# Kernel tuning notes

Measured on AMD Instinct MI355X. Metric: run time of the kernel, lower is better.

## Reference

```python
import jax, jax.numpy as jnp
import numpy as np
import math

HEAD_DIM = 128
NUM_HEADS = 16
ROPE_BASE = 10000.0


def _rope(x, st_pos):
    # x: [B, S, H, hd], interleaved even/odd rotation as in the torch module
    S, hd = x.shape[1], x.shape[3]
    theta = 1.0 / (ROPE_BASE ** (jnp.arange(0, hd, 2, dtype=jnp.float32) / hd))  # [hd/2]
    pos = jnp.arange(st_pos, st_pos + S, dtype=jnp.float32)[:, None]             # [S,1]
    ang = pos * theta                                                            # [S, hd/2]
    sin = jnp.sin(ang)[None, :, None, :]
    cos = jnp.cos(ang)[None, :, None, :]
    xe, xo = x[..., 0::2], x[..., 1::2]
    re = xe * cos - xo * sin
    ro = xe * sin + xo * cos
    # re-interleave: stack pairs then flatten last two dims
    return jnp.stack([re, ro], axis=-1).reshape(x.shape)


def setup_inputs() -> dict:
    key = jax.random.key(0)
    ks = jax.random.split(key, 6)
    B, S, D = 4, 2048, 2048
    scale = 1.0 / math.sqrt(D)
    x = jax.random.normal(ks[0], (B, S, D), dtype=jnp.float32)
    # causal additive mask (prefill)
    mask = jnp.where(jnp.tril(jnp.ones((S, S), dtype=bool)), 0.0, -1e9).astype(jnp.float32)
    Wq = jax.random.normal(ks[1], (D, NUM_HEADS * HEAD_DIM), dtype=jnp.float32) * scale
    Wk = jax.random.normal(ks[2], (D, NUM_HEADS * HEAD_DIM), dtype=jnp.float32) * scale
    Wv = jax.random.normal(ks[3], (D, NUM_HEADS * HEAD_DIM), dtype=jnp.float32) * scale
    Wo = jax.random.normal(ks[4], (NUM_HEADS * HEAD_DIM, D), dtype=jnp.float32) * scale
    return {"x": x, "mask": mask, "Wq": Wq, "Wk": Wk, "Wv": Wv, "Wo": Wo, "st_pos": 0}


def reference(x, mask, Wq, Wk, Wv, Wo, st_pos):
    B, S, D = x.shape
    H, hd = NUM_HEADS, HEAD_DIM
    q = (x @ Wq).reshape(B, S, H, hd)
    k = (x @ Wk).reshape(B, S, H, hd)
    v = (x @ Wv).reshape(B, S, H, hd)
    q = _rope(q, st_pos)
    k = _rope(k, st_pos)
    # st_pos=0 prefill: cache slice == current k, v; n_rep == 1 (n_kv_heads=num_heads)
    scores = jnp.einsum('bqhd,bkhd->bhqk', q, k) / math.sqrt(hd)
    if mask is not None:
        scores = scores + mask
    attn = jax.nn.softmax(scores, axis=-1)
    a = jnp.einsum('bhqk,bkhd->bqhd', attn, v).reshape(B, S, H * hd)
    return a @ Wo
```

## Files before the change

kernel.cpp:

```cpp
#include <hip/hip_runtime.h>
#include <hip/hip_fp16.h>

typedef _Float16 f16;
typedef __attribute__((ext_vector_type(2))) _Float16 f16x2;
typedef __attribute__((ext_vector_type(4))) _Float16 f16x4v;
typedef __attribute__((ext_vector_type(8))) _Float16 f16x8;
typedef __attribute__((ext_vector_type(4))) float f32x4;
typedef __attribute__((ext_vector_type(4))) int i32x4;

#define DEV __device__ __forceinline__

static constexpr int S_ = 2048;
static constexpr int D_ = 2048;
static constexpr int H_ = 16;
static constexpr int HD_ = 128;
static constexpr int B_ = 4;
static constexpr int QKV_ST = 6144;

typedef const __attribute__((address_space(1))) void* gptr_t;
typedef __attribute__((address_space(3))) void* lptr_t;

DEV void gl_lds16(const void* gsrc, void* lds) {
  __builtin_amdgcn_global_load_lds((gptr_t)gsrc, (lptr_t)lds, 16, 0, 0);
}

DEV int cvt_pk_i32(float a, float b) {
  return __builtin_bit_cast(int, __builtin_amdgcn_cvt_pkrtz(a, b));
}

__global__ __launch_bounds__(256) void cvt_f32_to_f16(const float* __restrict__ in,
                                                      f16* __restrict__ out, long n) {
  long i0 = ((long)blockIdx.x * 256 + threadIdx.x) * 4;
  long stride = (long)gridDim.x * 256 * 4;
  for (long i = i0; i < n; i += stride) {
    float4 v = *(const float4*)(in + i);
    f16x4v o;
    o[0] = (f16)v.x; o[1] = (f16)v.y; o[2] = (f16)v.z; o[3] = (f16)v.w;
    *(f16x4v*)(out + i) = o;
  }
}

__global__ __launch_bounds__(256) void wtrans4(const float* __restrict__ W0, const float* __restrict__ W1,
                                               const float* __restrict__ W2, const float* __restrict__ W3,
                                               f16* __restrict__ Wt) {
  __shared__ float tile[32][33];
  int wi = blockIdx.y;
  const float* W = wi == 0 ? W0 : wi == 1 ? W1 : wi == 2 ? W2 : W3;
  f16* dst = Wt + (size_t)wi * D_ * D_;
  int bx = blockIdx.x & 63, by = blockIdx.x >> 6;
  int r0 = by << 5, c0 = bx << 5;
  int tx = threadIdx.x & 31, ty = threadIdx.x >> 5;
#pragma unroll
  for (int i = 0; i < 4; i++) {
    int r = ty + i * 8;
    tile[r][tx] = W[(size_t)(r0 + r) * D_ + c0 + tx];
  }
  __syncthreads();
#pragma unroll
  for (int i = 0; i < 4; i++) {
    int r = ty + i * 8;
    dst[(size_t)(c0 + r) * D_ + r0 + tx] = (f16)tile[tx][r];
  }
}

DEV f16x8 lds_frag(const f16* half, int row, int s, int lg) {
  int byte = row * 128 + s * 64 + lg * 16;
  byte ^= (row & 7) << 4;
  return *(const f16x8*)((const char*)half + byte);
}

template <typename CT>
__global__ __launch_bounds__(512, 2) void gemm8(const f16* __restrict__ A, const f16* __restrict__ Bt,
                                                CT* __restrict__ C, int M, int N, int K,
                                                int lda, int ldc, long subB, long subC) {
  __shared__ alignas(16) f16 As[2][2][128 * 64];
  __shared__ alignas(16) f16 Bs[2][2][128 * 64];
  int nbx = N >> 8;
  int nwg = (M >> 8) * nbx;
  int bid = blockIdx.x;
  int wi = bid / nwg;
  int bidl = bid - wi * nwg;
  Bt += (size_t)wi * subB;
  C += (size_t)wi * subC;
  int wg = (bidl & 7) * (nwg >> 3) + (bidl >> 3);
  int bx = wg % nbx, by = wg / nbx;
  int tid = threadIdx.x, w = tid >> 6, l = tid & 63;
  int wm = w >> 2, wn = w & 3, lg = l >> 4, ln = l & 15;
  int nt = K >> 6;
  const f16* Ab = A + (size_t)(by * 256) * lda;
  const f16* Bb = Bt + (size_t)(bx * 256) * K;

  auto stageA = [&](const f16* src0, int kt, f16* dst) {
#pragma unroll
    for (int j = 0; j < 2; j++) {
      int c = j * 8 + w;
      int row = c * 8 + (l >> 3);
      int scol = ((l & 7) ^ (row & 7)) << 3;
      gl_lds16(src0 + (size_t)row * lda + kt * 64 + scol, (char*)dst + c * 1024);
    }
  };
  auto stageB = [&](const f16* src0, int kt, f16* dst) {
#pragma unroll
    for (int j = 0; j < 2; j++) {
      int c = j * 8 + w;
      int row = c * 8 + (l >> 3);
      int scol = ((l & 7) ^ (row & 7)) << 3;
      gl_lds16(src0 + (size_t)row * K + kt * 64 + scol, (char*)dst + c * 1024);
    }
  };

  f32x4 acc[8][4] = {};

  stageA(Ab, 0, As[0][0]);
  stageA(Ab + (size_t)128 * lda, 0, As[0][1]);
  stageB(Bb, 0, Bs[0][0]);
  stageB(Bb + (size_t)128 * K, 0, Bs[0][1]);
  if (nt > 1) {
    stageB(Bb, 1, Bs[1][0]);
    stageB(Bb + (size_t)128 * K, 1, Bs[1][1]);
  }

  for (int t = 0; t < nt; t++) {
    if (t + 2 < nt) asm volatile("s_waitcnt vmcnt(4)" ::: "memory");
    else            asm volatile("s_waitcnt vmcnt(0)" ::: "memory");
    __builtin_amdgcn_s_barrier();
    asm volatile("" ::: "memory");
    const f16* Ah = As[t & 1][wm];
    const f16* Bh = Bs[t & 1][wn >> 1];
    int br0 = (wn & 1) * 64;
    f16x8 a[4], b0[4], b1[4];
#pragma unroll
    for (int i = 0; i < 4; i++) a[i] = lds_frag(Ah, i * 16 + ln, 0, lg);
#pragma unroll
    for (int i = 0; i < 4; i++) b0[i] = lds_frag(Bh, br0 + i * 16 + ln, 0, lg);
    if (t + 1 < nt) stageA(Ab, t + 1, As[(t + 1) & 1][0]);
    __builtin_amdgcn_s_barrier();
    asm volatile("" ::: "memory");
    __builtin_amdgcn_s_setprio(1);
#pragma unroll
    for (int mi = 0; mi < 4; mi++)
#pragma unroll
      for (int ni = 0; ni < 4; ni++)
        acc[mi][ni] = __builtin_amdgcn_mfma_f32_16x16x32_f16(a[mi], b0[ni], acc[mi][ni], 0, 0, 0);
    __builtin_amdgcn_s_setprio(0);
    __builtin_amdgcn_s_barrier();
    asm volatile("" ::: "memory");
#pragma unroll
    for (int i = 0; i < 4; i++) a[i] = lds_frag(Ah, i * 16 + ln, 1, lg);
#pragma unroll
    for (int i = 0; i < 4; i++) b1[i] = lds_frag(Bh, br0 + i * 16 + ln, 1, lg);
    if (t + 1 < nt) stageA(Ab + (size_t)128 * lda, t + 1, As[(t + 1) & 1][1]);
    __builtin_amdgcn_s_barrier();
    asm volatile("" ::: "memory");
    __builtin_amdgcn_s_setprio(1);
#pragma unroll
    for (int mi = 0; mi < 4; mi++)
#pragma unroll
      for (int ni = 0; ni < 4; ni++)
        acc[mi][ni] = __builtin_amdgcn_mfma_f32_16x16x32_f16(a[mi], b1[ni], acc[mi][ni], 0, 0, 0);
    __builtin_amdgcn_s_setprio(0);
    __builtin_amdgcn_s_barrier();
    asm volatile("" ::: "memory");
#pragma unroll
    for (int i = 0; i < 4; i++) a[i] = lds_frag(Ah, 64 + i * 16 + ln, 0, lg);
    if (t + 2 < nt) stageB(Bb, t + 2, Bs[t & 1][0]);
    __builtin_amdgcn_s_barrier();
    asm volatile("" ::: "memory");
    __builtin_amdgcn_s_setprio(1);
#pragma unroll
    for (int mi = 0; mi < 4; mi++)
#pragma unroll
      for (int ni = 0; ni < 4; ni++)
        acc[mi + 4][ni] = __builtin_amdgcn_mfma_f32_16x16x32_f16(a[mi], b0[ni], acc[mi + 4][ni], 0, 0, 0);
    __builtin_amdgcn_s_setprio(0);
    __builtin_amdgcn_s_barrier();
    asm volatile("" ::: "memory");
#pragma unroll
    for (int i = 0; i < 4; i++) a[i] = lds_frag(Ah, 64 + i * 16 + ln, 1, lg);
    if (t + 2 < nt) stageB(Bb + (size_t)128 * K, t + 2, Bs[t & 1][1]);
    __builtin_amdgcn_s_barrier();
    asm volatile("" ::: "memory");
    __builtin_amdgcn_s_setprio(1);
#pragma unroll
    for (int mi = 0; mi < 4; mi++)
#pragma unroll
      for (int ni = 0; ni < 4; ni++)
        acc[mi + 4][ni] = __builtin_amdgcn_mfma_f32_16x16x32_f16(a[mi], b1[ni], acc[mi + 4][ni], 0, 0, 0);
    __builtin_amdgcn_s_setprio(0);
    __builtin_amdgcn_s_barrier();
    asm volatile("" ::: "memory");
  }

  int row0 = by * 256 + wm * 128;
  int col0 = bx * 256 + wn * 64;
#pragma unroll
  for (int mi = 0; mi < 8; mi++)
#pragma unroll
    for (int ni = 0; ni < 4; ni++)
#pragma unroll
      for (int r4 = 0; r4 < 4; r4++) {
        int row = row0 + mi * 16 + lg * 4 + r4;
        int col = col0 + ni * 16 + ln;
        float o = acc[mi][ni][r4];
        if constexpr (sizeof(CT) == 2) {
          float oo = __shfl_xor(o, 1);
          if (!(ln & 1)) {
            f16x2 pp; pp[0] = (f16)o; pp[1] = (f16)oo;
            *(f16x2*)(&C[(size_t)row * ldc + col]) = pp;
          }
        } else {
          C[(size_t)row * ldc + col] = o;
        }
      }
}

__global__ __launch_bounds__(256) void rope_table(float2* __restrict__ tab, const int* __restrict__ st) {
  int i = blockIdx.x * 256 + threadIdx.x;
  int s = i >> 6, j = i & 63;
  float theta = powf(10000.f, -(float)j / 64.f);
  float ang = (float)(s + st[0]) * theta;
  tab[i] = make_float2(cosf(ang), sinf(ang));
}

__global__ __launch_bounds__(256) void rope_apply_k(f16* __restrict__ QKV, const float2* __restrict__ tab,
                                                    long npairs) {
  long i0 = (long)blockIdx.x * 256 + threadIdx.x;
  long stride = (long)gridDim.x * 256;
  for (long p = i0; p < npairs; p += stride) {
    long row = p >> 10;
    int jp = (int)(p & 1023);
    int s = (int)(row & (S_ - 1));
    float2 cs = tab[s * 64 + (jp & 63)];
    f16* px = QKV + row * QKV_ST + 2048 + 2 * jp;
    f16x2 v = *(const f16x2*)px;
    float xe = (float)v[0], xo = (float)v[1];
    float re = xe * cs.x - xo * cs.y;
    float ro = xe * cs.y + xo * cs.x;
    f16x2 o; o[0] = (f16)re; o[1] = (f16)ro;
    *(f16x2*)px = o;
  }
}

__global__ __launch_bounds__(256) void vtrans2(const f16* __restrict__ QKV, f16* __restrict__ VT2) {
  __shared__ alignas(16) f16 tile[64 * 128];
  int t = blockIdx.x, bh = blockIdx.y, b = bh >> 4, h = bh & 15;
  int tid = threadIdx.x, w = tid >> 6, l = tid & 63, lg = l >> 4, ln = l & 15;
  const f16* src = QKV + (size_t)(b * S_ + t * 64) * QKV_ST + 4096 + h * HD_;
#pragma unroll
  for (int i = 0; i < 4; i++) {
    int idx = i * 256 + tid;
    int r = idx >> 4, c8 = idx & 15;
    int c8s = c8 ^ ((r >> 3) & 3);
    *(f16x8*)(&tile[r * 128 + c8s * 8]) = *(const f16x8*)(src + (size_t)r * QKV_ST + c8 * 8);
  }
  __syncthreads();
  f16* dst = VT2 + (size_t)(bh * 32 + t) * 16 * 512;
#pragma unroll
  for (int ci = 0; ci < 4; ci++) {
    int c = w * 4 + ci;
    int nj = c >> 1, kk = c & 1;
    f16x8 v;
#pragma unroll
    for (int e = 0; e < 8; e++) {
      int r = 16 * (2 * kk + (e >> 2)) + 4 * lg + (e & 3);
      int col = nj * 16 + ln;
      int c8s = (col >> 3) ^ ((r >> 3) & 3);
      v[e] = tile[r * 128 + c8s * 8 + (col & 7)];
    }
    *(f16x8*)(dst + (size_t)c * 512 + l * 8) = v;
  }
}

__global__ __launch_bounds__(512, 4) void attn(f16* __restrict__ QKV, const f16* __restrict__ VT2,
                                               const float2* __restrict__ tab) {
  __shared__ alignas(16) f16 kls[2][2][64 * 128];
  int id = blockIdx.x;
  int r8 = id & 7, j = id >> 3;
  int u = j & 7, g = j >> 3;
  int bh = r8 + (g << 3);
  int b = bh >> 4, h = bh & 15;
  int tid = threadIdx.x, w = tid >> 6, l = tid & 63, lg = l >> 4, ln = l & 15;

  const float QSCALE = 0.12751744910173355f;
  const f16* kp = QKV + (size_t)(b * S_) * QKV_ST + 2048 + h * HD_;
  const f16* vp2 = VT2 + (size_t)bh * 32 * 16 * 512;

  auto stageK = [&](int buf, int half, int kv0) {
#pragma unroll
    for (int jj = 0; jj < 2; jj++) {
      int i = jj * 8 + w;
      int byte = i * 1024 + 16 * l;
      int r = byte >> 8;
      int c = (((byte >> 4) & 15) - r) & 15;
      gl_lds16(kp + (size_t)(kv0 + r) * QKV_ST + c * 8, (char*)kls[buf][half] + i * 1024);
    }
  };

#pragma unroll 1
  for (int pi = 0; pi < 2; pi++) {
    int qsel = pi ? u : 15 - u;
    int q0 = qsel << 7;
    int qrow = q0 + w * 16 + ln;
    f16* qp = QKV + (size_t)(b * S_ + qrow) * QKV_ST + h * HD_;
    const float2* tq = tab + (size_t)qrow * 64;
    f16x8 qf[4];
#pragma unroll
    for (int kc = 0; kc < 4; kc++) {
      f16x8 q = *(const f16x8*)(qp + kc * 32 + lg * 8);
#pragma unroll
      for (int p = 0; p < 4; p++) {
        float2 cs = tq[kc * 16 + lg * 4 + p];
        float e0 = (float)q[2 * p], e1 = (float)q[2 * p + 1];
        q[2 * p] = (f16)((e0 * cs.x - e1 * cs.y) * QSCALE);
        q[2 * p + 1] = (f16)((e0 * cs.y + e1 * cs.x) * QSCALE);
      }
      qf[kc] = q;
    }

    float m = -1e30f, lsum = 0.f;
    f32x4 oacc[8] = {};

    int np = qsel + 1;
    int nt64 = 2 * qsel + 2;
    if (pi) __syncthreads();
    stageK(0, 0, 0);
    stageK(0, 1, 64);
#pragma unroll 1
    for (int p = 0; p < np; p++) {
      __syncthreads();
      if (p + 1 < np) {
        stageK((p + 1) & 1, 0, (2 * p + 2) << 6);
        stageK((p + 1) & 1, 1, (2 * p + 3) << 6);
      }
#pragma unroll 1
      for (int ii = 0; ii < 2; ii++) {
        int t = 2 * p + ii;
        int kv0 = t << 6;
        if (kv0 > q0 + w * 16 + 15) continue;
        const f16* kb = kls[p & 1][ii];
        const f16* vt = vp2 + (size_t)t * 16 * 512;

        f32x4 sf[4];
        __builtin_amdgcn_s_setprio(1);
#pragma unroll
        for (int ni = 0; ni < 4; ni++) {
          int n = ni * 16 + ln;
          f32x4 s = {0.f, 0.f, 0.f, 0.f};
#pragma unroll
          for (int kc = 0; kc < 4; kc++) {
            int mch = kc * 4 + lg;
            f16x8 kf = *(const f16x8*)(&kb[n * 128 + (((mch + n) & 15) << 3)]);
            s = __builtin_amdgcn_mfma_f32_16x16x32_f16(kf, qf[kc], s, 0, 0, 0);
          }
          sf[ni] = s;
        }
        __builtin_amdgcn_s_setprio(0);

        f16x8 vfa[8];
#pragma unroll
        for (int c = 0; c < 8; c++) vfa[c] = *(const f16x8*)(vt + c * 512 + l * 8);

        if (t >= nt64 - 2) {
#pragma unroll
          for (int ni = 0; ni < 4; ni++) {
            int kvg = kv0 + ni * 16 + lg * 4;
#pragma unroll
            for (int r4 = 0; r4 < 4; r4++)
              if (kvg + r4 > qrow) sf[ni][r4] = -1e30f;
          }
        }
        float pm = fmaxf(fmaxf(fmaxf(sf[0][0], sf[0][1]), fmaxf(sf[0][2], sf[0][3])),
                         fmaxf(fmaxf(sf[1][0], sf[1][1]), fmaxf(sf[1][2], sf[1][3])));
        pm = fmaxf(pm, fmaxf(fmaxf(fmaxf(sf[2][0], sf[2][1]), fmaxf(sf[2][2], sf[2][3])),
                             fmaxf(fmaxf(sf[3][0], sf[3][1]), fmaxf(sf[3][2], sf[3][3]))));
        pm = fmaxf(pm, __shfl_xor(pm, 16));
        pm = fmaxf(pm, __shfl_xor(pm, 32));
        float scl = 1.f;
        bool defer = __all(pm <= m + 8.f);
        if (!defer) {
          float mn = fmaxf(m, pm);
          scl = __builtin_amdgcn_exp2f(m - mn);
          m = mn;
        }
        float rsum = 0.f;
#pragma unroll
        for (int ni = 0; ni < 4; ni++)
#pragma unroll
          for (int r4 = 0; r4 < 4; r4++) {
            float pv = __builtin_amdgcn_exp2f(sf[ni][r4] - m);
            sf[ni][r4] = pv;
            rsum += pv;
          }
        lsum = lsum * scl + rsum;

        if (!defer) {
#pragma unroll
          for (int nj = 0; nj < 8; nj++)
#pragma unroll
            for (int r4 = 0; r4 < 4; r4++) oacc[nj][r4] *= scl;
        }

        f16x8 pa[2];
#pragma unroll
        for (int kk = 0; kk < 2; kk++) {
          i32x4 wv;
          wv.x = cvt_pk_i32(sf[2 * kk][0], sf[2 * kk][1]);
          wv.y = cvt_pk_i32(sf[2 * kk][2], sf[2 * kk][3]);
          wv.z = cvt_pk_i32(sf[2 * kk + 1][0], sf[2 * kk + 1][1]);
          wv.w = cvt_pk_i32(sf[2 * kk + 1][2], sf[2 * kk + 1][3]);
          pa[kk] = __builtin_bit_cast(f16x8, wv);
        }

        __builtin_amdgcn_s_setprio(1);
#pragma unroll
        for (int kk = 0; kk < 2; kk++)
#pragma unroll
          for (int nj = 0; nj < 4; nj++)
            oacc[nj] = __builtin_amdgcn_mfma_f32_16x16x32_f16(vfa[nj * 2 + kk], pa[kk], oacc[nj], 0, 0, 0);
#pragma unroll
        for (int njb = 0; njb < 2; njb++) {
          f16x8 vf[4];
#pragma unroll
          for (int jj = 0; jj < 2; jj++)
#pragma unroll
            for (int kk = 0; kk < 2; kk++)
              vf[jj * 2 + kk] = *(const f16x8*)(vt + (size_t)(((4 + njb * 2 + jj) * 2 + kk) * 512) + l * 8);
#pragma unroll
          for (int kk = 0; kk < 2; kk++)
#pragma unroll
            for (int jj = 0; jj < 2; jj++)
              oacc[4 + njb * 2 + jj] = __builtin_amdgcn_mfma_f32_16x16x32_f16(
                  vf[jj * 2 + kk], pa[kk], oacc[4 + njb * 2 + jj], 0, 0, 0);
        }
        __builtin_amdgcn_s_setprio(0);
      }
    }

    lsum += __shfl_xor(lsum, 16);
    lsum += __shfl_xor(lsum, 32);
    float inv = 1.f / lsum;
#pragma unroll
    for (int nj = 0; nj < 8; nj++) {
      f16x4v ov;
#pragma unroll
      for (int r4 = 0; r4 < 4; r4++) ov[r4] = (f16)(oacc[nj][r4] * inv);
      *(f16x4v*)(qp + nj * 16 + lg * 4) = ov;
    }
  }
}

extern "C" void kernel_launch(void* const* d_in, const int* in_sizes, int n_in,
                              void* d_out, int out_size, void* d_ws, size_t ws_size,
                              hipStream_t stream) {
  (void)in_sizes; (void)n_in; (void)out_size; (void)ws_size;
  const float* x = (const float*)d_in[0];
  const float* Wq = (const float*)d_in[2];
  const float* Wk = (const float*)d_in[3];
  const float* Wv = (const float*)d_in[4];
  const float* Wo = (const float*)d_in[5];
  const int* stp = (const int*)d_in[6];
  float* out = (float*)d_out;

  const size_t MS = (size_t)B_ * S_;
  f16* xh = (f16*)d_ws;
  f16* wqt = xh + MS * D_;
  f16* wot = wqt + (size_t)3 * D_ * D_;
  f16* qkv = wot + (size_t)D_ * D_;
  float2* tab = (float2*)(qkv + MS * (size_t)QKV_ST);
  f16* vt2 = xh;

  cvt_f32_to_f16<<<16384, 256, 0, stream>>>(x, xh, (long)(MS * D_));
  wtrans4<<<dim3(4096, 4), 256, 0, stream>>>(Wq, Wk, Wv, Wo, wqt);
  gemm8<f16><<<768, 512, 0, stream>>>(xh, wqt, qkv, 8192, 2048, 2048, 2048, QKV_ST,
                                      (long)D_ * D_, 2048);
  rope_table<<<512, 256, 0, stream>>>(tab, stp);
  rope_apply_k<<<4096, 256, 0, stream>>>(qkv, tab, (long)(MS * 1024));
  vtrans2<<<dim3(32, 64), 256, 0, stream>>>(qkv, vt2);
  attn<<<512, 512, 0, stream>>>(qkv, vt2, tab);
  gemm8<float><<<256, 512, 0, stream>>>(qkv, wot, out, 8192, 2048, 2048, QKV_ST, 2048, 0, 0);
}
```

Before: 451.9 us.

## Merge GEMM main-loop phases into two halves with fewer barriers

The GEMM main loop is reorganised from four compute phases, each fenced by two workgroup barriers, into two phases. Both B fragments and both A row-halves are loaded up front, the next A tile is staged in one group, and interleaved MFMAs update all eight accumulator rows per phase. The aim is to cut barrier stalls and give the scheduler longer uninterrupted MFMA runs. The cost is more live fragment registers, which may raise VGPR pressure or reduce occupancy.

```diff
diff --git a/kernel.cpp b/kernel.cpp
--- a/kernel.cpp
+++ b/kernel.cpp
@@ -128,66 +128,47 @@
     const f16* Ah = As[t & 1][wm];
     const f16* Bh = Bs[t & 1][wn >> 1];
     int br0 = (wn & 1) * 64;
-    f16x8 a[4], b0[4], b1[4];
-#pragma unroll
-    for (int i = 0; i < 4; i++) a[i] = lds_frag(Ah, i * 16 + ln, 0, lg);
+    f16x8 alo[4], ahi[4], b0[4], b1[4];
 #pragma unroll
     for (int i = 0; i < 4; i++) b0[i] = lds_frag(Bh, br0 + i * 16 + ln, 0, lg);
-    if (t + 1 < nt) stageA(Ab, t + 1, As[(t + 1) & 1][0]);
-    __builtin_amdgcn_s_barrier();
-    asm volatile("" ::: "memory");
+#pragma unroll
+    for (int i = 0; i < 4; i++) b1[i] = lds_frag(Bh, br0 + i * 16 + ln, 1, lg);
+#pragma unroll
+    for (int i = 0; i < 4; i++) alo[i] = lds_frag(Ah, i * 16 + ln, 0, lg);
+#pragma unroll
+    for (int i = 0; i < 4; i++) ahi[i] = lds_frag(Ah, 64 + i * 16 + ln, 0, lg);
+    if (t + 1 < nt) {
+      stageA(Ab, t + 1, As[(t + 1) & 1][0]);
+      stageA(Ab + (size_t)128 * lda, t + 1, As[(t + 1) & 1][1]);
+    }
     __builtin_amdgcn_s_setprio(1);
 #pragma unroll
     for (int mi = 0; mi < 4; mi++)
 #pragma unroll
-      for (int ni = 0; ni < 4; ni++)
-        acc[mi][ni] = __builtin_amdgcn_mfma_f32_16x16x32_f16(a[mi], b0[ni], acc[mi][ni], 0, 0, 0);
+      for (int ni = 0; ni < 4; ni++) {
+        acc[mi][ni] = __builtin_amdgcn_mfma_f32_16x16x32_f16(alo[mi], b0[ni], acc[mi][ni], 0, 0, 0);
+        acc[mi + 4][ni] = __builtin_amdgcn_mfma_f32_16x16x32_f16(ahi[mi], b0[ni], acc[mi + 4][ni], 0, 0, 0);
+      }
     __builtin_amdgcn_s_setprio(0);
     __builtin_amdgcn_s_barrier();
     asm volatile("" ::: "memory");
 #pragma unroll
-    for (int i = 0; i < 4; i++) a[i] = lds_frag(Ah, i * 16 + ln, 1, lg);
-#pragma unroll
-    for (int i = 0; i < 4; i++) b1[i] = lds_frag(Bh, br0 + i * 16 + ln, 1, lg);
-    if (t + 1 < nt) stageA(Ab + (size_t)128 * lda, t + 1, As[(t + 1) & 1][1]);
-    __builtin_amdgcn_s_barrier();
-    asm volatile("" ::: "memory");
+    for (int i = 0; i < 4; i++) alo[i] = lds_frag(Ah, i * 16 + ln, 1, lg);
+#pragma unroll
+    for (int i = 0; i < 4; i++) ahi[i] = lds_frag(Ah, 64 + i * 16 + ln, 1, lg);
+    if (t + 2 < nt) {
+      stageB(Bb, t + 2, Bs[t & 1][0]);
+      stageB(Bb + (size_t)128 * K, t + 2, Bs[t & 1][1]);
+    }
     __builtin_amdgcn_s_setprio(1);
 #pragma unroll
     for (int mi = 0; mi < 4; mi++)
 #pragma unroll
-      for (int ni = 0; ni < 4; ni++)
-        acc[mi][ni] = __builtin_amdgcn_mfma_f32_16x16x32_f16(a[mi], b1[ni], acc[mi][ni], 0, 0, 0);
+      for (int ni = 0; ni < 4; ni++) {
+        acc[mi][ni] = __builtin_amdgcn_mfma_f32_16x16x32_f16(alo[mi], b1[ni], acc[mi][ni], 0, 0, 0);
+        acc[mi + 4][ni] = __builtin_amdgcn_mfma_f32_16x16x32_f16(ahi[mi], b1[ni], acc[mi + 4][ni], 0, 0, 0);
+      }
     __builtin_amdgcn_s_setprio(0);
-    __builtin_amdgcn_s_barrier();
-    asm volatile("" ::: "memory");
-#pragma unroll
-    for (int i = 0; i < 4; i++) a[i] = lds_frag(Ah, 64 + i * 16 + ln, 0, lg);
-    if (t + 2 < nt) stageB(Bb, t + 2, Bs[t & 1][0]);
-    __builtin_amdgcn_s_barrier();
-    asm volatile("" ::: "memory");
-    __builtin_amdgcn_s_setprio(1);
-#pragma unroll
-    for (int mi = 0; mi < 4; mi++)
-#pragma unroll
-      for (int ni = 0; ni < 4; ni++)
-        acc[mi + 4][ni] = __builtin_amdgcn_mfma_f32_16x16x32_f16(a[mi], b0[ni], acc[mi + 4][ni], 0, 0, 0);
-    __builtin_amdgcn_s_setprio(0);
-    __builtin_amdgcn_s_barrier();
-    asm volatile("" ::: "memory");
-#pragma unroll
-    for (int i = 0; i < 4; i++) a[i] = lds_frag(Ah, 64 + i * 16 + ln, 1, lg);
-    if (t + 2 < nt) stageB(Bb + (size_t)128 * K, t + 2, Bs[t & 1][1]);
-    __builtin_amdgcn_s_barrier();
-    asm volatile("" ::: "memory");
-    __builtin_amdgcn_s_setprio(1);
-#pragma unroll
-    for (int mi = 0; mi < 4; mi++)
-#pragma unroll
-      for (int ni = 0; ni < 4; ni++)
-        acc[mi + 4][ni] = __builtin_amdgcn_mfma_f32_16x16x32_f16(a[mi], b1[ni], acc[mi + 4][ni], 0, 0, 0);
-    __builtin_amdgcn_s_setprio(0);
-    __builtin_amdgcn_s_barrier();
     asm volatile("" ::: "memory");
   }
 
```

Measured after the change: 436.8 us. 3.3% less time.
